# Performance work log

Hardware: AMD Instinct MI355X
Metric: run time of the kernel (lower is better)

Reference implementation:

```python
import jax, jax.numpy as jnp
import numpy as np

# ---- MjCambrianEyeConfig constants ----
RES = (128, 128)              # sensor resolution (pixels)
SENSOR = (0.01, 0.01)         # sensor size Lx, Ly (meters)
APERTURE_OPEN = 0.5           # fraction of max aperture
FOCAL = 0.05                  # propagation distance z2 = config.focal[0] (meters)
WAVELENGTHS = (610e-9, 530e-9, 470e-9)  # R, G, B (meters)


def _rs_prop(u1, z, FX, FY, lmbda):
    # Rayleigh-Sommerfeld transfer-function propagation.
    k = 2.0 * np.pi / lmbda
    arg = 1.0 - (lmbda * FX) ** 2 - (lmbda * FY) ** 2  # (My, Mx)
    valid = jnp.sqrt(FX ** 2 + FY ** 2) < 1.0 / lmbda   # matches H_valid; arg>0 <=> valid
    H = jnp.where(valid, jnp.exp(1j * (k * z) * jnp.sqrt(jnp.where(arg > 0, arg, 0.0))), 0.0)
    U1 = jnp.fft.fft2(jnp.fft.fftshift(u1))
    U2 = jnp.fft.fftshift(H) * U1
    return jnp.fft.ifftshift(jnp.fft.ifft2(U2))


def _simple_psf(depth):
    Mx, My = RES[0] * 2, RES[1] * 2
    if Mx % 2 == 0:
        Mx += 1
    if My % 2 == 0:
        My += 1
    Lx, Ly = SENSOR
    dx, dy = Lx / Mx, Ly / My
    x1 = jnp.linspace(-Lx / 2.0, Lx / 2.0, Mx)
    y1 = jnp.linspace(-Ly / 2.0, Ly / 2.0, My)
    X1, Y1 = jnp.meshgrid(x1, y1)                         # (My, Mx)
    fx = jnp.linspace(-1.0 / (2.0 * dx), 1.0 / (2.0 * dx), Mx)
    fy = jnp.linspace(-1.0 / (2.0 * dy), 1.0 / (2.0 * dy), My)
    FX, FY = jnp.meshgrid(fx, fy)
    ap_radius = float(np.clip(APERTURE_OPEN, 0.0, 1.0)) * dx * (Mx // 2)
    R2 = X1 ** 2 + Y1 ** 2
    A = (jnp.sqrt(R2) / (ap_radius + 1e-7) <= 1.0).astype(jnp.float32)  # aperture mask
    z1 = jnp.mean(depth)
    psfs = []
    for lam in WAVELENGTHS:  # small fixed loop over 3 wavelengths
        k = 2.0 * np.pi / lam
        u = jnp.exp(1j * k * jnp.sqrt(R2 + z1 ** 2)) * A  # spherical wave at aperture
        u = _rs_prop(u, FOCAL, FX, FY, lam)
        psf = jnp.abs(u) ** 2
        psfs.append(psf / (jnp.sum(psf) + 1e-7))
    return jnp.stack(psfs, axis=-1).astype(jnp.float32)  # (My, Mx, 3)


def setup_inputs() -> dict:
    key = jax.random.key(0)
    k1, k2 = jax.random.split(key)
    image = jax.random.uniform(k1, (128, 128, 3), dtype=jnp.float32)
    depth = jax.random.uniform(k2, (128, 128), dtype=jnp.float32)
    return {"image": image, "depth": depth}


def reference(image, depth):
    psf = _simple_psf(depth)                       # (My, Mx, 3)
    lhs = jnp.transpose(image, (2, 0, 1))[None]    # (1, 3, H, W)
    rhs = jnp.transpose(psf, (2, 0, 1))[:, None]   # (3, 1, Kh, Kw)
    # Per-channel 'same' cross-correlation == torch conv2d per channel
    out = jax.lax.conv_general_dilated(lhs, rhs, window_strides=(1, 1), padding='SAME', feature_group_count=3)
    img = jnp.transpose(out[0], (1, 2, 0))         # (H, W, 3)
    return img, psf
```

## Files before the change

### kernel.cpp

```cpp
#include <hip/hip_runtime.h>
#include <math.h>

#define NN 257
#define NN2 66049
#define PROW 260
#define PCH (PROW * NN)
#define NRZ 17
#define FSW 288

#define SWG(f) (((((f) >> 2) ^ (((f) >> 5) & 7)) << 2))
#define SW(f) (SWG(f) | ((f) & 3))

static const double D_PI = 3.14159265358979323846;

__device__ __forceinline__ double lam_of(int c) {
    return c == 0 ? 610e-9 : (c == 1 ? 530e-9 : 470e-9);
}

__device__ __forceinline__ float2 phase_of(double rev) {
    rev -= floor(rev);
    float ang = (float)(2.0 * D_PI * rev);
    float sv, cv;
    __sincosf(ang, &sv, &cv);
    return make_float2(cv, sv);
}

template <int SIGN, int MODE>
__global__ __launch_bounds__(256) void k_dft(const float2* __restrict__ in, float2* __restrict__ out,
                                             const float* __restrict__ depth,
                                             float* __restrict__ raw, double* __restrict__ sums) {
    __shared__ float4 col[NN];
    __shared__ float2 twL[NN];
    __shared__ float4 sacc2[3][64][2];
    __shared__ float4 red[4];
    const int ah = blockIdx.x;
    const int by = blockIdx.y;
    const int c = blockIdx.z;
    int bc0, bc1;
    if (MODE == 0 || MODE == 3) {
        bc0 = (by < 64) ? 2 * by : 256;
        bc1 = (by < 64) ? bc0 + 1 : 256;
    } else if (MODE == 1) {
        bc0 = (by < 64) ? 2 * by : 128;
        bc1 = (by < 64) ? bc0 + 1 : 128;
    } else {
        bc0 = 2 * by;
        bc1 = (bc0 < 256) ? bc0 + 1 : 256;
    }
    const float dupf = (bc1 == bc0) ? 0.f : 1.f;
    const int tid = threadIdx.x;

    if (MODE == 2) {
        if (ah == 0 && by == 0 && tid == 0) sums[c] = 0.0;
    }

    for (int t = tid; t < NN; t += 256) {
        double th = 2.0 * D_PI * (double)t / 257.0;
        double sv, cv; sincos(th, &sv, &cv);
        twL[t] = make_float2((float)cv, (float)(-sv));
    }

    double z1 = 0.0;
    if (MODE == 0) {
        double* sred = (double*)sacc2;
        double acc = 0.0;
        for (int i = tid; i < 16384; i += 256) acc += (double)depth[i];
        sred[tid] = acc;
        __syncthreads();
        for (int o = 128; o > 0; o >>= 1) {
            if (tid < o) sred[tid] += sred[tid + o];
            __syncthreads();
        }
        z1 = sred[0] / 16384.0;
        __syncthreads();
    }

    for (int t = tid; t < NN; t += 256) {
        float2 v0, v1;
        if (MODE == 0) {
            int js = t + 129; if (js >= NN) js -= NN;
            const double step = 0.01 / 256.0;
            double yy = -0.005 + js * step;
            double lam = lam_of(c);
            const double ap = 0.5 * (0.01 / 257.0) * 128.0 + 1e-7;
            {
                int is = bc0 + 129; if (is >= NN) is -= NN;
                double x = -0.005 + is * step;
                double r2 = x * x + yy * yy;
                v0 = make_float2(0.f, 0.f);
                if (sqrt(r2) <= ap) v0 = phase_of(sqrt(r2 + z1 * z1) / lam);
            }
            {
                int is = bc1 + 129; if (is >= NN) is -= NN;
                double x = -0.005 + is * step;
                double r2 = x * x + yy * yy;
                v1 = make_float2(0.f, 0.f);
                if (sqrt(r2) <= ap) v1 = phase_of(sqrt(r2 + z1 * z1) / lam);
            }
        } else {
            v0 = in[(c * NN + t) * NN + bc0];
            v1 = in[(c * NN + t) * NN + bc1];
            if (MODE == 2) {
                int ps = t + 129; if (ps >= NN) ps -= NN;
                const double fstep = 25700.0 / 256.0;
                double fy = -12850.0 + ps * fstep;
                double lam = lam_of(c);
                double ilam2 = 1.0 / (lam * lam);
                double kzr = 0.05 / lam;
                {
                    int qs = bc0 + 129; if (qs >= NN) qs -= NN;
                    double fx = -12850.0 + qs * fstep;
                    double lfx = lam * fx, lfy = lam * fy;
                    double a2 = 1.0 - lfx * lfx - lfy * lfy;
                    float2 hh = make_float2(0.f, 0.f);
                    if (fx * fx + fy * fy < ilam2) hh = phase_of(kzr * sqrt(a2 > 0.0 ? a2 : 0.0));
                    v0 = make_float2(v0.x * hh.x - v0.y * hh.y, v0.x * hh.y + v0.y * hh.x);
                }
                {
                    int qs = bc1 + 129; if (qs >= NN) qs -= NN;
                    double fx = -12850.0 + qs * fstep;
                    double lfx = lam * fx, lfy = lam * fy;
                    double a2 = 1.0 - lfx * lfx - lfy * lfy;
                    float2 hh = make_float2(0.f, 0.f);
                    if (fx * fx + fy * fy < ilam2) hh = phase_of(kzr * sqrt(a2 > 0.0 ? a2 : 0.0));
                    v1 = make_float2(v1.x * hh.x - v1.y * hh.y, v1.x * hh.y + v1.y * hh.x);
                }
            }
        }
        col[t] = make_float4(v0.x, v0.y, v1.x, v1.y);
    }
    __syncthreads();

    const float invn4 = (float)(1.0 / ((double)NN2 * (double)NN2));
    const int q = tid >> 6;
    const int al = tid & 63;
    int aval[2];
    aval[0] = ah * 128 + al;
    aval[1] = aval[0] + 64;

    float cx[2][4], cy[2][4], wx[2], wy[2];
    #pragma unroll
    for (int aa = 0; aa < 2; ++aa) {
        #pragma unroll
        for (int m = 0; m < 4; ++m) {
            int sm = (aval[aa] * (q + 4 * m)) % 257;
            float2 tt = twL[sm];
            cx[aa][m] = tt.x; cy[aa][m] = -SIGN * tt.y;
        }
        float2 w16 = twL[(16 * aval[aa]) % 257];
        wx[aa] = w16.x; wy[aa] = -SIGN * w16.y;
    }

    float AX0[2] = {0.f, 0.f}, AY0[2] = {0.f, 0.f}, BX0[2] = {0.f, 0.f}, BY0[2] = {0.f, 0.f};
    float AX1[2] = {0.f, 0.f}, AY1[2] = {0.f, 0.f}, BX1[2] = {0.f, 0.f}, BY1[2] = {0.f, 0.f};

    for (int j = 0; j < 16; ++j) {
        const int tbase = q + 16 * j;
        #pragma unroll
        for (int m = 0; m < 4; ++m) {
            float4 v = col[tbase + 4 * m];
            #pragma unroll
            for (int aa = 0; aa < 2; ++aa) {
                float cxr = cx[aa][m], cyr = cy[aa][m];
                if (m < 2) {
                    AX0[aa] = fmaf(v.x, cxr, AX0[aa]); AX0[aa] = fmaf(-v.y, cyr, AX0[aa]);
                    AY0[aa] = fmaf(v.x, cyr, AY0[aa]); AY0[aa] = fmaf(v.y, cxr, AY0[aa]);
                    BX0[aa] = fmaf(v.z, cxr, BX0[aa]); BX0[aa] = fmaf(-v.w, cyr, BX0[aa]);
                    BY0[aa] = fmaf(v.z, cyr, BY0[aa]); BY0[aa] = fmaf(v.w, cxr, BY0[aa]);
                } else {
                    AX1[aa] = fmaf(v.x, cxr, AX1[aa]); AX1[aa] = fmaf(-v.y, cyr, AX1[aa]);
                    AY1[aa] = fmaf(v.x, cyr, AY1[aa]); AY1[aa] = fmaf(v.y, cxr, AY1[aa]);
                    BX1[aa] = fmaf(v.z, cxr, BX1[aa]); BX1[aa] = fmaf(-v.w, cyr, BX1[aa]);
                    BY1[aa] = fmaf(v.z, cyr, BY1[aa]); BY1[aa] = fmaf(v.w, cxr, BY1[aa]);
                }
                float nx = fmaf(cxr, wx[aa], -cyr * wy[aa]);
                float ny = fmaf(cxr, wy[aa], cyr * wx[aa]);
                cx[aa][m] = nx; cy[aa][m] = ny;
            }
        }
    }

    float ax0[2], ay0[2], ax1[2], ay1[2];
    #pragma unroll
    for (int aa = 0; aa < 2; ++aa) {
        ax0[aa] = AX0[aa] + AX1[aa]; ay0[aa] = AY0[aa] + AY1[aa];
        ax1[aa] = BX0[aa] + BX1[aa]; ay1[aa] = BY0[aa] + BY1[aa];
    }

    if (q == 0) {
        float4 v = col[256];
        #pragma unroll
        for (int aa = 0; aa < 2; ++aa) {
            float2 tb = twL[aval[aa]];
            float ex = tb.x, ey = SIGN * tb.y;
            ax0[aa] = fmaf(v.x, ex, ax0[aa]); ax0[aa] = fmaf(-v.y, ey, ax0[aa]);
            ay0[aa] = fmaf(v.x, ey, ay0[aa]); ay0[aa] = fmaf(v.y, ex, ay0[aa]);
            ax1[aa] = fmaf(v.z, ex, ax1[aa]); ax1[aa] = fmaf(-v.w, ey, ax1[aa]);
            ay1[aa] = fmaf(v.z, ey, ay1[aa]); ay1[aa] = fmaf(v.w, ex, ay1[aa]);
        }
    } else {
        #pragma unroll
        for (int aa = 0; aa < 2; ++aa)
            sacc2[q - 1][al][aa] = make_float4(ax0[aa], ay0[aa], ax1[aa], ay1[aa]);
    }
    __syncthreads();

    const bool mv0 = (MODE == 0) ? (bc0 <= 127) : (bc0 >= 1 && bc0 <= 128);
    const bool mv1 = ((MODE == 0) ? (bc1 <= 127) : (bc1 >= 1 && bc1 <= 128)) && (bc1 != bc0);
    const int bm0 = (MODE == 0) ? (255 - bc0) : (257 - bc0);
    const int bm1 = (MODE == 0) ? (255 - bc1) : (257 - bc1);
    const bool pm = (MODE == 3) && (bc0 <= 127);

    double sum_local = 0.0;
    if (q == 0) {
        #pragma unroll
        for (int aa = 0; aa < 2; ++aa) {
            #pragma unroll
            for (int r = 0; r < 3; ++r) {
                float4 b = sacc2[r][al][aa];
                ax0[aa] += b.x; ay0[aa] += b.y; ax1[aa] += b.z; ay1[aa] += b.w;
            }
            if (MODE < 3) {
                out[(c * NN + bc0) * NN + aval[aa]] = make_float2(ax0[aa], ay0[aa]);
                out[(c * NN + bc1) * NN + aval[aa]] = make_float2(ax1[aa], ay1[aa]);
                if (MODE < 2) {
                    const int a = aval[aa];
                    const int am = (a == 0) ? 0 : (257 - a);
                    if (mv0) {
                        int m = 2 * a + ((MODE == 1) ? 2 * bc0 : 0);
                        m %= 257;
                        float fx = twL[m].x, fy = -SIGN * twL[m].y;
                        out[(c * NN + bm0) * NN + am] =
                            make_float2(ax0[aa] * fx - ay0[aa] * fy, ax0[aa] * fy + ay0[aa] * fx);
                    }
                    if (mv1) {
                        int m = 2 * a + ((MODE == 1) ? 2 * bc1 : 0);
                        m %= 257;
                        float fx = twL[m].x, fy = -SIGN * twL[m].y;
                        out[(c * NN + bm1) * NN + am] =
                            make_float2(ax1[aa] * fx - ay1[aa] * fy, ax1[aa] * fy + ay1[aa] * fx);
                    }
                }
            } else {
                int jj0 = bc0 + 129; if (jj0 >= NN) jj0 -= NN;
                int jj1 = bc1 + 129; if (jj1 >= NN) jj1 -= NN;
                int ii = aval[aa] + 129; if (ii >= NN) ii -= NN;
                float m0 = fmaf(ax0[aa], ax0[aa], ay0[aa] * ay0[aa]) * invn4;
                float m1 = fmaf(ax1[aa], ax1[aa], ay1[aa] * ay1[aa]) * invn4;
                raw[c * PCH + jj0 * PROW + ii] = m0;
                raw[c * PCH + jj1 * PROW + ii] = m1;
                sum_local += (double)m0 + (double)(dupf * m1);
                if (pm) {
                    int im = 256 - ii;
                    raw[c * PCH + (256 - jj0) * PROW + im] = m0;
                    raw[c * PCH + (256 - jj1) * PROW + im] = m1;
                    sum_local += (double)m0 + (double)(dupf * m1);
                }
            }
        }
    }

    if (ah == (int)gridDim.x - 1) {
        float c_ = twL[tid].x, s_ = SIGN * twL[tid].y;
        float4 cv = col[tid];
        float tx0 = cv.x * c_ - cv.y * s_;
        float ty0 = cv.x * s_ + cv.y * c_;
        float tx1 = cv.z * c_ - cv.w * s_;
        float ty1 = cv.z * s_ + cv.w * c_;
        if (tid == 0) {
            c_ = twL[256].x; s_ = SIGN * twL[256].y;
            cv = col[256];
            tx0 += cv.x * c_ - cv.y * s_;
            ty0 += cv.x * s_ + cv.y * c_;
            tx1 += cv.z * c_ - cv.w * s_;
            ty1 += cv.z * s_ + cv.w * c_;
        }
        for (int o = 32; o > 0; o >>= 1) {
            tx0 += __shfl_down(tx0, o);
            ty0 += __shfl_down(ty0, o);
            tx1 += __shfl_down(tx1, o);
            ty1 += __shfl_down(ty1, o);
        }
        int wid = tid >> 6;
        if ((tid & 63) == 0) red[wid] = make_float4(tx0, ty0, tx1, ty1);
        __syncthreads();
        if (tid == 0) {
            float Xx0 = red[0].x + red[1].x + red[2].x + red[3].x;
            float Xy0 = red[0].y + red[1].y + red[2].y + red[3].y;
            float Xx1 = red[0].z + red[1].z + red[2].z + red[3].z;
            float Xy1 = red[0].w + red[1].w + red[2].w + red[3].w;
            if (MODE < 3) {
                out[(c * NN + bc0) * NN + 256] = make_float2(Xx0, Xy0);
                out[(c * NN + bc1) * NN + 256] = make_float2(Xx1, Xy1);
                if (MODE < 2) {
                    if (mv0) {
                        int m = 512 + ((MODE == 1) ? 2 * bc0 : 0);
                        m %= 257;
                        float fx = twL[m].x, fy = -SIGN * twL[m].y;
                        out[(c * NN + bm0) * NN + 1] = make_float2(Xx0 * fx - Xy0 * fy, Xx0 * fy + Xy0 * fx);
                    }
                    if (mv1) {
                        int m = 512 + ((MODE == 1) ? 2 * bc1 : 0);
                        m %= 257;
                        float fx = twL[m].x, fy = -SIGN * twL[m].y;
                        out[(c * NN + bm1) * NN + 1] = make_float2(Xx1 * fx - Xy1 * fy, Xx1 * fy + Xy1 * fx);
                    }
                }
            } else {
                int jj0 = bc0 + 129; if (jj0 >= NN) jj0 -= NN;
                int jj1 = bc1 + 129; if (jj1 >= NN) jj1 -= NN;
                float m0 = fmaf(Xx0, Xx0, Xy0 * Xy0) * invn4;
                float m1 = fmaf(Xx1, Xx1, Xy1 * Xy1) * invn4;
                raw[c * PCH + jj0 * PROW + 128] = m0;
                raw[c * PCH + jj1 * PROW + 128] = m1;
                sum_local += (double)m0 + (double)(dupf * m1);
                if (pm) {
                    raw[c * PCH + (256 - jj0) * PROW + 128] = m0;
                    raw[c * PCH + (256 - jj1) * PROW + 128] = m1;
                    sum_local += (double)m0 + (double)(dupf * m1);
                }
            }
        }
    }

    if (MODE == 3) {
        if (tid < 64) {
            double s = sum_local;
            for (int o = 32; o > 0; o >>= 1) s += __shfl_down(s, o);
            if (tid == 0) atomicAdd(&sums[c], s);
        }
    }
}

#define CM16(A, P, Q, iv)                                                                                   \
    A.x = fmaf(iv.x, Q.x, A.x); A.x = fmaf(iv.y, P.w, A.x); A.x = fmaf(iv.z, P.z, A.x); A.x = fmaf(iv.w, P.y, A.x); \
    A.y = fmaf(iv.x, Q.y, A.y); A.y = fmaf(iv.y, Q.x, A.y); A.y = fmaf(iv.z, P.w, A.y); A.y = fmaf(iv.w, P.z, A.y); \
    A.z = fmaf(iv.x, Q.z, A.z); A.z = fmaf(iv.y, Q.y, A.z); A.z = fmaf(iv.z, Q.x, A.z); A.z = fmaf(iv.w, P.w, A.z); \
    A.w = fmaf(iv.x, Q.w, A.w); A.w = fmaf(iv.y, Q.z, A.w); A.w = fmaf(iv.z, Q.y, A.w); A.w = fmaf(iv.w, Q.x, A.w);

__global__ __launch_bounds__(256) void k_conv(const float* __restrict__ img, const float* __restrict__ psf,
                                              float* __restrict__ part) {
    __shared__ float F[8][FSW];
    __shared__ float simg[15][132];
    __shared__ float sacc[3][4][260];
    const int yt = blockIdx.x;
    const int rz = blockIdx.y;
    const int c = blockIdx.z;
    const int y0 = yt * 8;
    const int r0 = 121 - y0 + 8 * rz;
    const int tid = threadIdx.x;
    const int tx = tid & 7;
    const int ty = (tid >> 3) & 7;
    const int rh = tid >> 6;
    const int x0 = 16 * tx;
    const int ulo = 8 * rz - 7;

    for (int g = tid; g < 8 * 65; g += 256) {
        int rr = g / 65, q = g - 65 * rr;
        const float* G = psf + c * PCH + (r0 + rr) * PROW + 4 * q;
        float4 A = *(const float4*)G;
        if (q < 64) {
            F[rr][SW(256 - 4 * q)] = A.x;
            F[rr][SW(255 - 4 * q)] = A.y;
            F[rr][SW(254 - 4 * q)] = A.z;
            F[rr][SW(253 - 4 * q)] = A.w;
        } else {
            F[rr][SW(0)] = A.x;
        }
    }
    for (int g = tid; g < 15 * 32; g += 256) {
        int rw = g >> 5, q = g & 31;
        int u = ulo + rw;
        float4 v = make_float4(0.f, 0.f, 0.f, 0.f);
        if (u >= 0 && u < 128) {
            const float* I = img + (u * 128 + 4 * q) * 3 + c;
            v = make_float4(I[0], I[3], I[6], I[9]);
        }
        *(float4*)&simg[rw][4 * q] = v;
    }
    __syncthreads();

    float4 A0 = make_float4(0.f, 0.f, 0.f, 0.f), A1 = A0, A2 = A0, A3 = A0;

    #pragma unroll
    for (int rr2 = 0; rr2 < 2; ++rr2) {
        const int rr = 2 * rh + rr2;
        const float* Fr = &F[rr][0];
        const float* I = &simg[ty + rr][0];
        float4 W0c = *(const float4*)(Fr + SWG(x0 + 128));
        float4 W1c = *(const float4*)(Fr + SWG(x0 + 132));
        float4 W2c = *(const float4*)(Fr + SWG(x0 + 136));
        float4 W3c = *(const float4*)(Fr + SWG(x0 + 140));
        #pragma unroll 2
        for (int vb = 0; vb < 128; vb += 4) {
            float4 Wm1 = *(const float4*)(Fr + SWG(x0 + 124 - vb));
            float4 iv = *(const float4*)(I + vb);
            CM16(A0, Wm1, W0c, iv)
            CM16(A1, W0c, W1c, iv)
            CM16(A2, W1c, W2c, iv)
            CM16(A3, W2c, W3c, iv)
            W3c = W2c; W2c = W1c; W1c = W0c; W0c = Wm1;
        }
    }

    if (rh != 0) {
        int s = tid & 63;
        *(float4*)&sacc[rh - 1][0][4 * s] = A0;
        *(float4*)&sacc[rh - 1][1][4 * s] = A1;
        *(float4*)&sacc[rh - 1][2][4 * s] = A2;
        *(float4*)&sacc[rh - 1][3][4 * s] = A3;
    }
    __syncthreads();
    if (rh == 0) {
        int s = tid;
        #pragma unroll
        for (int r = 0; r < 3; ++r) {
            float4 b0 = *(const float4*)&sacc[r][0][4 * s];
            float4 b1 = *(const float4*)&sacc[r][1][4 * s];
            float4 b2 = *(const float4*)&sacc[r][2][4 * s];
            float4 b3 = *(const float4*)&sacc[r][3][4 * s];
            A0.x += b0.x; A0.y += b0.y; A0.z += b0.z; A0.w += b0.w;
            A1.x += b1.x; A1.y += b1.y; A1.z += b1.z; A1.w += b1.w;
            A2.x += b2.x; A2.y += b2.y; A2.z += b2.z; A2.w += b2.w;
            A3.x += b3.x; A3.y += b3.y; A3.z += b3.z; A3.w += b3.w;
        }
        const int y = y0 + ty;
        float* dst = part + ((rz * 3 + c) * 128 + y) * 128 + x0;
        *(float4*)dst = A0;
        *(float4*)(dst + 4) = A1;
        *(float4*)(dst + 8) = A2;
        *(float4*)(dst + 12) = A3;
    }
}

__global__ __launch_bounds__(256) void k_final(const float* __restrict__ part, const float* __restrict__ raw,
                                               const double* __restrict__ sums, float* __restrict__ out) {
    int gid = blockIdx.x * 256 + threadIdx.x;
    if (gid < 49152) {
        int c = gid >> 14;
        int r = gid & 16383;
        float s = 0.f;
        #pragma unroll
        for (int rz = 0; rz < NRZ; ++rz) s += part[((rz * 3 + c) * 128 + (r >> 7)) * 128 + (r & 127)];
        float inv = (float)(1.0 / (sums[c] + 1e-7));
        out[r * 3 + c] = s * inv;
    } else {
        int o = gid - 49152;
        if (o < 3 * NN2) {
            int idx = o / 3, c = o - 3 * idx;
            int j = idx / NN, i = idx - NN * j;
            float inv = (float)(1.0 / (sums[c] + 1e-7));
            out[49152 + o] = raw[c * PCH + j * PROW + i] * inv;
        }
    }
}

extern "C" void kernel_launch(void* const* d_in, const int* in_sizes, int n_in,
                              void* d_out, int out_size, void* d_ws, size_t ws_size,
                              hipStream_t stream) {
    const float* img = (const float*)d_in[0];
    const float* depth = (const float*)d_in[1];
    float* out = (float*)d_out;

    char* ws = (char*)d_ws;
    double* zsums = (double*)ws;
    float2* bufA = (float2*)(ws + 64);
    float2* bufB = bufA + 3 * NN2;
    float* raw = (float*)(bufB + 3 * NN2);
    float* part = raw + 3 * PCH;

    k_dft<-1, 0><<<dim3(2, 65, 3), 256, 0, stream>>>(nullptr, bufA, depth, nullptr, nullptr);
    k_dft<-1, 1><<<dim3(2, 65, 3), 256, 0, stream>>>(bufA, bufB, nullptr, nullptr, nullptr);
    k_dft< 1, 2><<<dim3(1, 129, 3), 256, 0, stream>>>(bufB, bufA, nullptr, nullptr, zsums);
    k_dft< 1, 3><<<dim3(2, 65, 3), 256, 0, stream>>>(bufA, nullptr, nullptr, raw, zsums);
    k_conv<<<dim3(16, NRZ, 3), 256, 0, stream>>>(img, raw, part);
    k_final<<<(49152 + 3 * NN2 + 255) / 256, 256, 0, stream>>>(part, raw, zsums, out);
}
```

Before: 83.07 us.

## Fuse final reduction into conv via atomics and transpose DFT intermediate layout

Removes the k_final kernel. Each conv block now scales its partial sum by the PSF normalization and atomically adds it into a zero-initialized output image. An extra block column writes the normalized PSF output. Separately, the DFT stages read and write intermediates transposed, changing which index is contiguous in memory. This saves one launch and the partial-buffer round trip, at the cost of float atomic contention across 17 z-slices, a memset, and nondeterministic summation order.

```diff
diff --git a/kernel.cpp b/kernel.cpp
--- a/kernel.cpp
+++ b/kernel.cpp
@@ -98,8 +98,8 @@
                 if (sqrt(r2) <= ap) v1 = phase_of(sqrt(r2 + z1 * z1) / lam);
             }
         } else {
-            v0 = in[(c * NN + t) * NN + bc0];
-            v1 = in[(c * NN + t) * NN + bc1];
+            v0 = in[(c * NN + bc0) * NN + t];
+            v1 = in[(c * NN + bc1) * NN + t];
             if (MODE == 2) {
                 int ps = t + 129; if (ps >= NN) ps -= NN;
                 const double fstep = 25700.0 / 256.0;
@@ -221,8 +221,8 @@
                 ax0[aa] += b.x; ay0[aa] += b.y; ax1[aa] += b.z; ay1[aa] += b.w;
             }
             if (MODE < 3) {
-                out[(c * NN + bc0) * NN + aval[aa]] = make_float2(ax0[aa], ay0[aa]);
-                out[(c * NN + bc1) * NN + aval[aa]] = make_float2(ax1[aa], ay1[aa]);
+                out[(c * NN + aval[aa]) * NN + bc0] = make_float2(ax0[aa], ay0[aa]);
+                out[(c * NN + aval[aa]) * NN + bc1] = make_float2(ax1[aa], ay1[aa]);
                 if (MODE < 2) {
                     const int a = aval[aa];
                     const int am = (a == 0) ? 0 : (257 - a);
@@ -230,14 +230,14 @@
                         int m = 2 * a + ((MODE == 1) ? 2 * bc0 : 0);
                         m %= 257;
                         float fx = twL[m].x, fy = -SIGN * twL[m].y;
-                        out[(c * NN + bm0) * NN + am] =
+                        out[(c * NN + am) * NN + bm0] =
                             make_float2(ax0[aa] * fx - ay0[aa] * fy, ax0[aa] * fy + ay0[aa] * fx);
                     }
                     if (mv1) {
                         int m = 2 * a + ((MODE == 1) ? 2 * bc1 : 0);
                         m %= 257;
                         float fx = twL[m].x, fy = -SIGN * twL[m].y;
-                        out[(c * NN + bm1) * NN + am] =
+                        out[(c * NN + am) * NN + bm1] =
                             make_float2(ax1[aa] * fx - ay1[aa] * fy, ax1[aa] * fy + ay1[aa] * fx);
                     }
                 }
@@ -290,20 +290,20 @@
             float Xx1 = red[0].z + red[1].z + red[2].z + red[3].z;
             float Xy1 = red[0].w + red[1].w + red[2].w + red[3].w;
             if (MODE < 3) {
-                out[(c * NN + bc0) * NN + 256] = make_float2(Xx0, Xy0);
-                out[(c * NN + bc1) * NN + 256] = make_float2(Xx1, Xy1);
+                out[(c * NN + 256) * NN + bc0] = make_float2(Xx0, Xy0);
+                out[(c * NN + 256) * NN + bc1] = make_float2(Xx1, Xy1);
                 if (MODE < 2) {
                     if (mv0) {
                         int m = 512 + ((MODE == 1) ? 2 * bc0 : 0);
                         m %= 257;
                         float fx = twL[m].x, fy = -SIGN * twL[m].y;
-                        out[(c * NN + bm0) * NN + 1] = make_float2(Xx0 * fx - Xy0 * fy, Xx0 * fy + Xy0 * fx);
+                        out[(c * NN + 1) * NN + bm0] = make_float2(Xx0 * fx - Xy0 * fy, Xx0 * fy + Xy0 * fx);
                     }
                     if (mv1) {
                         int m = 512 + ((MODE == 1) ? 2 * bc1 : 0);
                         m %= 257;
                         float fx = twL[m].x, fy = -SIGN * twL[m].y;
-                        out[(c * NN + bm1) * NN + 1] = make_float2(Xx1 * fx - Xy1 * fy, Xx1 * fy + Xy1 * fx);
+                        out[(c * NN + 1) * NN + bm1] = make_float2(Xx1 * fx - Xy1 * fy, Xx1 * fy + Xy1 * fx);
                     }
                 }
             } else {
@@ -339,16 +339,30 @@
     A.w = fmaf(iv.x, Q.w, A.w); A.w = fmaf(iv.y, Q.z, A.w); A.w = fmaf(iv.z, Q.y, A.w); A.w = fmaf(iv.w, Q.x, A.w);
 
 __global__ __launch_bounds__(256) void k_conv(const float* __restrict__ img, const float* __restrict__ psf,
-                                              float* __restrict__ part) {
+                                              const double* __restrict__ sums, float* __restrict__ out) {
     __shared__ float F[8][FSW];
     __shared__ float simg[15][132];
     __shared__ float sacc[3][4][260];
     const int yt = blockIdx.x;
     const int rz = blockIdx.y;
     const int c = blockIdx.z;
+    const int tid = threadIdx.x;
+    const float inv = (float)(1.0 / (sums[c] + 1e-7));
+
+    if (yt == 16) {
+        #pragma unroll
+        for (int k = 0; k < 16; ++k) {
+            int e = rz * 256 + tid + k * (NRZ * 256);
+            if (e < NN2) {
+                int j = e / NN, i = e - j * NN;
+                out[49152 + e * 3 + c] = psf[c * PCH + j * PROW + i] * inv;
+            }
+        }
+        return;
+    }
+
     const int y0 = yt * 8;
     const int r0 = 121 - y0 + 8 * rz;
-    const int tid = threadIdx.x;
     const int tx = tid & 7;
     const int ty = (tid >> 3) & 7;
     const int rh = tid >> 6;
@@ -425,33 +439,15 @@
             A3.x += b3.x; A3.y += b3.y; A3.z += b3.z; A3.w += b3.w;
         }
         const int y = y0 + ty;
-        float* dst = part + ((rz * 3 + c) * 128 + y) * 128 + x0;
-        *(float4*)dst = A0;
-        *(float4*)(dst + 4) = A1;
-        *(float4*)(dst + 8) = A2;
-        *(float4*)(dst + 12) = A3;
-    }
-}
-
-__global__ __launch_bounds__(256) void k_final(const float* __restrict__ part, const float* __restrict__ raw,
-                                               const double* __restrict__ sums, float* __restrict__ out) {
-    int gid = blockIdx.x * 256 + threadIdx.x;
-    if (gid < 49152) {
-        int c = gid >> 14;
-        int r = gid & 16383;
-        float s = 0.f;
-        #pragma unroll
-        for (int rz = 0; rz < NRZ; ++rz) s += part[((rz * 3 + c) * 128 + (r >> 7)) * 128 + (r & 127)];
-        float inv = (float)(1.0 / (sums[c] + 1e-7));
-        out[r * 3 + c] = s * inv;
-    } else {
-        int o = gid - 49152;
-        if (o < 3 * NN2) {
-            int idx = o / 3, c = o - 3 * idx;
-            int j = idx / NN, i = idx - NN * j;
-            float inv = (float)(1.0 / (sums[c] + 1e-7));
-            out[49152 + o] = raw[c * PCH + j * PROW + i] * inv;
-        }
+        float* dst = out + (y * 128 + x0) * 3 + c;
+        atomicAdd(&dst[0],  A0.x * inv); atomicAdd(&dst[3],  A0.y * inv);
+        atomicAdd(&dst[6],  A0.z * inv); atomicAdd(&dst[9],  A0.w * inv);
+        atomicAdd(&dst[12], A1.x * inv); atomicAdd(&dst[15], A1.y * inv);
+        atomicAdd(&dst[18], A1.z * inv); atomicAdd(&dst[21], A1.w * inv);
+        atomicAdd(&dst[24], A2.x * inv); atomicAdd(&dst[27], A2.y * inv);
+        atomicAdd(&dst[30], A2.z * inv); atomicAdd(&dst[33], A2.w * inv);
+        atomicAdd(&dst[36], A3.x * inv); atomicAdd(&dst[39], A3.y * inv);
+        atomicAdd(&dst[42], A3.z * inv); atomicAdd(&dst[45], A3.w * inv);
     }
 }
 
@@ -467,12 +463,11 @@
     float2* bufA = (float2*)(ws + 64);
     float2* bufB = bufA + 3 * NN2;
     float* raw = (float*)(bufB + 3 * NN2);
-    float* part = raw + 3 * PCH;
-
+
+    hipMemsetAsync(out, 0, 49152 * sizeof(float), stream);
     k_dft<-1, 0><<<dim3(2, 65, 3), 256, 0, stream>>>(nullptr, bufA, depth, nullptr, nullptr);
     k_dft<-1, 1><<<dim3(2, 65, 3), 256, 0, stream>>>(bufA, bufB, nullptr, nullptr, nullptr);
     k_dft< 1, 2><<<dim3(1, 129, 3), 256, 0, stream>>>(bufB, bufA, nullptr, nullptr, zsums);
     k_dft< 1, 3><<<dim3(2, 65, 3), 256, 0, stream>>>(bufA, nullptr, nullptr, raw, zsums);
-    k_conv<<<dim3(16, NRZ, 3), 256, 0, stream>>>(img, raw, part);
-    k_final<<<(49152 + 3 * NN2 + 255) / 256, 256, 0, stream>>>(part, raw, zsums, out);
+    k_conv<<<dim3(17, NRZ, 3), 256, 0, stream>>>(img, raw, zsums, out);
 }
```

Measured after the change: 107.3 us. 29.2% more time.
